# Kernel optimization log

Measured on AMD Instinct MI355X. Metric: run time of the kernel, lower is better.

Reference implementation:

```python
import jax, jax.numpy as jnp
import numpy as np

USERNUM = 8192
ITEMNUM = 8192
DIM = 256
EPS_NORM = 1e-8   # torch.cosine_similarity default eps
CLAMP_MIN = 1e-6
CLAMP_MAX = 1.0


def setup_inputs() -> dict:
    key = jax.random.key(0)
    ks = jax.random.split(key, 12)
    N = USERNUM + ITEMNUM
    s = 1.0 / np.sqrt(DIM)
    return {
        "A": jax.random.uniform(ks[0], (N, N), dtype=jnp.float32) * (2.0 / N),
        "features": jax.random.normal(ks[1], (N, DIM), dtype=jnp.float32),
        "Wg": jax.random.normal(ks[2], (DIM, DIM), dtype=jnp.float32) * s,
        "bg": jnp.zeros((DIM,), dtype=jnp.float32),
        "uW1": jax.random.normal(ks[3], (DIM, DIM), dtype=jnp.float32) * s,
        "ub1": jnp.zeros((DIM,), dtype=jnp.float32),
        "uW2": jax.random.normal(ks[4], (DIM, DIM), dtype=jnp.float32) * s,
        "ub2": jnp.zeros((DIM,), dtype=jnp.float32),
        "iW1": jax.random.normal(ks[5], (DIM, DIM), dtype=jnp.float32) * s,
        "ib1": jnp.zeros((DIM,), dtype=jnp.float32),
        "iW2": jax.random.normal(ks[6], (DIM, DIM), dtype=jnp.float32) * s,
        "ib2": jnp.zeros((DIM,), dtype=jnp.float32),
    }


def _mlp(h, W1, b1, W2, b2):
    return jax.nn.relu(h @ W1 + b1) @ W2 + b2


def reference(A, features, Wg, bg, uW1, ub1, uW2, ub2, iW1, ib1, iW2, ib2):
    # GCN layer: relu(A @ X @ W + b)  -> [N, DIM]
    x = jax.nn.relu((A @ features) @ Wg + bg)
    user = x[:USERNUM]
    item = x[USERNUM:]
    u = _mlp(user, uW1, ub1, uW2, ub2)   # [usernum, DIM]
    it = _mlp(item, iW1, ib1, iW2, ib2)  # [itemnum, DIM]
    # Fused L2-normalize + GEMM replaces the per-row cosine_similarity loop.
    un = u / jnp.maximum(jnp.linalg.norm(u, axis=1, keepdims=True), EPS_NORM)
    itn = it / jnp.maximum(jnp.linalg.norm(it, axis=1, keepdims=True), EPS_NORM)
    sim = un @ itn.T                      # [usernum, itemnum]
    return jnp.clip(sim, CLAMP_MIN, CLAMP_MAX)
```

## Files before the change

### kernel.cpp

```cpp
#include <hip/hip_runtime.h>
#include <hip/hip_bf16.h>

using f32x4 = __attribute__((ext_vector_type(4))) float;
using s16x8 = __attribute__((ext_vector_type(8))) short;
using i32x4 = __attribute__((ext_vector_type(4))) int;

#define NTOT 16384
#define NUSER 8192
#define DIM 256

__device__ __forceinline__ unsigned short f2bf(float f) {
  union { float f; unsigned u; } v; v.f = f;
  unsigned r = v.u + 0x7FFFu + ((v.u >> 16) & 1u);
  return (unsigned short)(r >> 16);
}

__device__ __forceinline__ unsigned pack2bf(float x, float y) {
  float2 t; t.x = x; t.y = y;
  __hip_bfloat162 h = __float22bfloat162_rn(t);
  union { __hip_bfloat162 h; unsigned u; } cv; cv.h = h;
  return cv.u;
}

__device__ __forceinline__ void gload_lds16(const void* g, void* l) {
  __builtin_amdgcn_global_load_lds(
      (const __attribute__((address_space(1))) unsigned int*)g,
      (__attribute__((address_space(3))) unsigned int*)l, 16, 0, 0);
}

__global__ __launch_bounds__(256) void transpose_cvt(const float* __restrict__ src,
                                                     unsigned short* __restrict__ dst,
                                                     int K, int N) {
  __shared__ float tile[64][65];
  const int k0 = blockIdx.x * 64, n0 = blockIdx.y * 64;
  const int t = threadIdx.x;
#pragma unroll
  for (int i = 0; i < 16; i++) {
    int idx = i * 256 + t, r = idx >> 6, c = idx & 63;
    tile[r][c] = src[(size_t)(k0 + r) * N + n0 + c];
  }
  __syncthreads();
#pragma unroll
  for (int i = 0; i < 16; i++) {
    int idx = i * 256 + t, r = idx >> 6, c = idx & 63;
    dst[(size_t)(n0 + r) * K + k0 + c] = f2bf(tile[c][r]);
  }
}

__global__ __launch_bounds__(256) void transpose_w5(const float* __restrict__ w0,
                                                    const float* __restrict__ w1,
                                                    const float* __restrict__ w2,
                                                    const float* __restrict__ w3,
                                                    const float* __restrict__ w4,
                                                    unsigned short* __restrict__ dstbase) {
  __shared__ float tile[64][65];
  const float* srcs[5] = {w0, w1, w2, w3, w4};
  const float* src = srcs[blockIdx.z];
  unsigned short* dst = dstbase + (size_t)blockIdx.z * 65536;
  const int k0 = blockIdx.x * 64, n0 = blockIdx.y * 64;
  const int t = threadIdx.x;
#pragma unroll
  for (int i = 0; i < 16; i++) {
    int idx = i * 256 + t, r = idx >> 6, c = idx & 63;
    tile[r][c] = src[(size_t)(k0 + r) * 256 + n0 + c];
  }
  __syncthreads();
#pragma unroll
  for (int i = 0; i < 16; i++) {
    int idx = i * 256 + t, r = idx >> 6, c = idx & 63;
    dst[(size_t)(n0 + r) * 256 + k0 + c] = f2bf(tile[c][r]);
  }
}

__global__ __launch_bounds__(512) void gemm1(const float* __restrict__ A,
                                             const unsigned short* __restrict__ Ft,
                                             float* __restrict__ F1p) {
  __shared__ char smem[144 * 1024];
  char* const Ab0 = smem;
  char* const Ab1 = smem + 16 * 1024;
  char* const Ab2 = smem + 32 * 1024;
  char* const Bb0 = smem + 48 * 1024;
  char* const Bb1 = smem + 80 * 1024;
  char* const Bb2 = smem + 112 * 1024;

  const int tid = threadIdx.x;
  const int l = tid & 63, w = tid >> 6;
  const int wm = w >> 2, wn = w & 3;
  const int lr = l & 15, lk = l >> 4;

  const int lin = blockIdx.x;
  const int xcd = lin & 7, slot = lin >> 3;
  const int ks = xcd >> 2;
  const int mblk = (xcd & 3) * 32 + slot;
  const int m0 = mblk * 128;
  const size_t ks0 = (size_t)ks * 8192;
  float* out = F1p + (size_t)ks * NTOT * DIM;

  const int arow = tid >> 4, ac16 = tid & 15;
  const float* asrc = A + (size_t)(m0 + arow) * NTOT + ks0 + ac16 * 4;
  int aoff[4];
#pragma unroll
  for (int j = 0; j < 4; j++) {
    int r = j * 32 + arow;
    aoff[j] = r * 128 + ((ac16 * 8) ^ ((r & 7) << 4));
  }

  const int brin = l >> 3;
  const int bldso = w * 4096;
  const char* bsrc = (const char*)Ft + (size_t)(w * 32 + brin) * (NTOT * 2) +
                     ks0 * 2 + (((l & 7) * 16) ^ (brin << 4));

  f32x4 zero = {0.f, 0.f, 0.f, 0.f};
  f32x4 acc[4][4];
#pragma unroll
  for (int i = 0; i < 4; i++)
#pragma unroll
    for (int j = 0; j < 4; j++) acc[i][j] = zero;

  struct AQuad { f32x4 v[4]; };
  AQuad av0, av1, av2;

  auto issueB = [&](int t, char* Bb) {
#pragma unroll
    for (int i = 0; i < 4; i++)
      gload_lds16(bsrc + (size_t)i * 8 * (NTOT * 2) + t * 128,
                  Bb + bldso + i * 1024);
  };
  auto loadA = [&](int t, AQuad& s) {
#pragma unroll
    for (int j = 0; j < 4; j++)
      s.v[j] = __builtin_nontemporal_load(
          (const f32x4*)(asrc + (size_t)j * 32 * NTOT + t * 64));
  };
  auto writeA = [&](const AQuad& s, char* Ab) {
#pragma unroll
    for (int j = 0; j < 4; j++) {
      unsigned lo = pack2bf(s.v[j].x, s.v[j].y);
      unsigned hi = pack2bf(s.v[j].z, s.v[j].w);
      *(unsigned long long*)(Ab + aoff[j]) =
          (unsigned long long)lo | ((unsigned long long)hi << 32);
    }
  };
  auto compute = [&](const char* Ab, const char* Bb) {
#pragma unroll
    for (int kh = 0; kh < 2; kh++) {
      s16x8 af[4], bf[4];
#pragma unroll
      for (int mt = 0; mt < 4; mt++) {
        int r = wm * 64 + mt * 16 + lr;
        int off = r * 128 + ((kh * 64 + lk * 16) ^ ((r & 7) << 4));
        af[mt] = *(const s16x8*)(Ab + off);
      }
#pragma unroll
      for (int nt = 0; nt < 4; nt++) {
        int n = wn * 64 + nt * 16 + lr;
        int off = n * 128 + ((kh * 64 + lk * 16) ^ ((n & 7) << 4));
        bf[nt] = *(const s16x8*)(Bb + off);
      }
#pragma unroll
      for (int mt = 0; mt < 4; mt++)
#pragma unroll
        for (int nt = 0; nt < 4; nt++)
          acc[mt][nt] = __builtin_amdgcn_mfma_f32_16x16x32_bf16(af[mt], bf[nt],
                                                                acc[mt][nt], 0, 0, 0);
    }
  };

#define STEP_BAR(N)                                                \
  asm volatile("s_waitcnt vmcnt(" #N ") lgkmcnt(0)" ::: "memory"); \
  __builtin_amdgcn_s_barrier();                                    \
  __builtin_amdgcn_sched_barrier(0);

  issueB(0, Bb0);
  loadA(0, av0);
  issueB(1, Bb1);
  loadA(1, av1);
  writeA(av0, Ab0);
  STEP_BAR(8)

  for (int t = 0; t < 126; t += 3) {
    issueB(t + 2, Bb2);
    loadA(t + 2, av2);
    compute(Ab0, Bb0);
    writeA(av1, Ab1);
    STEP_BAR(8)
    issueB(t + 3, Bb0);
    loadA(t + 3, av0);
    compute(Ab1, Bb1);
    writeA(av2, Ab2);
    STEP_BAR(8)
    issueB(t + 4, Bb1);
    loadA(t + 4, av1);
    compute(Ab2, Bb2);
    writeA(av0, Ab0);
    STEP_BAR(8)
  }
  compute(Ab0, Bb0);
  writeA(av1, Ab1);
  STEP_BAR(0)
  compute(Ab1, Bb1);
#undef STEP_BAR

#pragma unroll
  for (int mt = 0; mt < 4; mt++) {
    int rbase = m0 + wm * 64 + mt * 16 + lk * 4;
#pragma unroll
    for (int nt = 0; nt < 4; nt++) {
      int c = wn * 64 + nt * 16 + lr;
#pragma unroll
      for (int j = 0; j < 4; j++)
        __builtin_nontemporal_store(acc[mt][nt][j],
                                    out + (size_t)(rbase + j) * DIM + c);
    }
  }
}

__global__ __launch_bounds__(512) void mlp_in(const float* __restrict__ P,
                                              const unsigned short* __restrict__ WT,
                                              const float* __restrict__ bias,
                                              unsigned short* __restrict__ out) {
  __shared__ char smem[40 * 1024];
  char* Ab = smem;
  char* Bb = smem + 8 * 1024;
  const int tid = threadIdx.x, l = tid & 63, w = tid >> 6;
  const int wm = w >> 2, wn = w & 3;
  const int m0 = blockIdx.x * 64;
  const int arow = tid >> 4, ac4 = tid & 15;
  const int bn = tid >> 3, bg = tid & 7;
  const int lr = l & 15, lk = l >> 4;

  f32x4 zero = {0.f, 0.f, 0.f, 0.f};
  f32x4 acc[2][4];
#pragma unroll
  for (int i = 0; i < 2; i++)
#pragma unroll
    for (int j = 0; j < 4; j++) acc[i][j] = zero;

  for (int step = 0; step < 4; step++) {
#pragma unroll
    for (int i = 0; i < 2; i++) {
      int r = i * 32 + arow;
      size_t gi = (size_t)(m0 + r) * DIM + step * 64 + ac4 * 4;
      f32x4 v = *(const f32x4*)(P + gi);
      v += *(const f32x4*)(P + (size_t)NTOT * DIM + gi);
      unsigned lo = pack2bf(v.x, v.y);
      unsigned hi = pack2bf(v.z, v.w);
      int off = (r * 128 + ac4 * 8) ^ ((r & 7) << 4);
      *(unsigned long long*)(Ab + off) =
          (unsigned long long)lo | ((unsigned long long)hi << 32);
    }
#pragma unroll
    for (int i = 0; i < 4; i++) {
      int n = i * 64 + bn;
      i32x4 v = *(const i32x4*)(WT + (size_t)n * DIM + step * 64 + bg * 8);
      int off = (n * 128 + bg * 16) ^ ((n & 7) << 4);
      *(i32x4*)(Bb + off) = v;
    }
    __syncthreads();
#pragma unroll
    for (int kh = 0; kh < 2; kh++) {
      s16x8 af[2], bfr[4];
#pragma unroll
      for (int mt = 0; mt < 2; mt++) {
        int r = wm * 32 + mt * 16 + lr;
        int off = (r * 128 + kh * 64 + lk * 16) ^ ((r & 7) << 4);
        af[mt] = *(const s16x8*)(Ab + off);
      }
#pragma unroll
      for (int nt = 0; nt < 4; nt++) {
        int n = wn * 64 + nt * 16 + lr;
        int off = (n * 128 + kh * 64 + lk * 16) ^ ((n & 7) << 4);
        bfr[nt] = *(const s16x8*)(Bb + off);
      }
#pragma unroll
      for (int mt = 0; mt < 2; mt++)
#pragma unroll
        for (int nt = 0; nt < 4; nt++)
          acc[mt][nt] = __builtin_amdgcn_mfma_f32_16x16x32_bf16(af[mt], bfr[nt],
                                                                acc[mt][nt], 0, 0, 0);
    }
    __syncthreads();
  }
#pragma unroll
  for (int nt = 0; nt < 4; nt++) {
    int c = wn * 64 + nt * 16 + lr;
    float b = bias[c];
#pragma unroll
    for (int mt = 0; mt < 2; mt++) {
      int rbase = m0 + wm * 32 + mt * 16 + lk * 4;
#pragma unroll
      for (int j = 0; j < 4; j++) {
        float v = fmaxf(acc[mt][nt][j] + b, 0.f);
        out[(size_t)(rbase + j) * DIM + c] = f2bf(v);
      }
    }
  }
}

__global__ __launch_bounds__(512) void mlp_hidden(const unsigned short* __restrict__ X,
                                                  const unsigned short* __restrict__ WTu,
                                                  const unsigned short* __restrict__ WTi,
                                                  const float* __restrict__ bu,
                                                  const float* __restrict__ bi,
                                                  unsigned short* __restrict__ out) {
  __shared__ char smem[40 * 1024];
  char* Ab = smem;
  char* Bb = smem + 8 * 1024;
  const int tid = threadIdx.x, l = tid & 63, w = tid >> 6;
  const int wm = w >> 2, wn = w & 3;
  const int m0 = blockIdx.x * 64;
  const unsigned short* WT = (m0 < NUSER) ? WTu : WTi;
  const float* bias = (m0 < NUSER) ? bu : bi;
  const int ar = tid >> 3, ag = tid & 7;
  const int bn = tid >> 3, bg = tid & 7;
  const int lr = l & 15, lk = l >> 4;

  f32x4 zero = {0.f, 0.f, 0.f, 0.f};
  f32x4 acc[2][4];
#pragma unroll
  for (int i = 0; i < 2; i++)
#pragma unroll
    for (int j = 0; j < 4; j++) acc[i][j] = zero;

  for (int step = 0; step < 4; step++) {
    {
      i32x4 v = *(const i32x4*)(X + (size_t)(m0 + ar) * DIM + step * 64 + ag * 8);
      int off = (ar * 128 + ag * 16) ^ ((ar & 7) << 4);
      *(i32x4*)(Ab + off) = v;
    }
#pragma unroll
    for (int i = 0; i < 4; i++) {
      int n = i * 64 + bn;
      i32x4 v = *(const i32x4*)(WT + (size_t)n * DIM + step * 64 + bg * 8);
      int off = (n * 128 + bg * 16) ^ ((n & 7) << 4);
      *(i32x4*)(Bb + off) = v;
    }
    __syncthreads();
#pragma unroll
    for (int kh = 0; kh < 2; kh++) {
      s16x8 af[2], bfr[4];
#pragma unroll
      for (int mt = 0; mt < 2; mt++) {
        int r = wm * 32 + mt * 16 + lr;
        int off = (r * 128 + kh * 64 + lk * 16) ^ ((r & 7) << 4);
        af[mt] = *(const s16x8*)(Ab + off);
      }
#pragma unroll
      for (int nt = 0; nt < 4; nt++) {
        int n = wn * 64 + nt * 16 + lr;
        int off = (n * 128 + kh * 64 + lk * 16) ^ ((n & 7) << 4);
        bfr[nt] = *(const s16x8*)(Bb + off);
      }
#pragma unroll
      for (int mt = 0; mt < 2; mt++)
#pragma unroll
        for (int nt = 0; nt < 4; nt++)
          acc[mt][nt] = __builtin_amdgcn_mfma_f32_16x16x32_bf16(af[mt], bfr[nt],
                                                                acc[mt][nt], 0, 0, 0);
    }
    __syncthreads();
  }
#pragma unroll
  for (int nt = 0; nt < 4; nt++) {
    int c = wn * 64 + nt * 16 + lr;
    float b = bias[c];
#pragma unroll
    for (int mt = 0; mt < 2; mt++) {
      int rbase = m0 + wm * 32 + mt * 16 + lk * 4;
#pragma unroll
      for (int j = 0; j < 4; j++) {
        float v = fmaxf(acc[mt][nt][j] + b, 0.f);
        out[(size_t)(rbase + j) * DIM + c] = f2bf(v);
      }
    }
  }
}

__global__ __launch_bounds__(512) void mlp_out_norm(const unsigned short* __restrict__ H,
                                                    const unsigned short* __restrict__ WTu,
                                                    const unsigned short* __restrict__ WTi,
                                                    const float* __restrict__ bu,
                                                    const float* __restrict__ bi,
                                                    unsigned short* __restrict__ un) {
  __shared__ char smem[40 * 1024];
  __shared__ float rs[64][4];
  char* Ab = smem;
  char* Bb = smem + 8 * 1024;
  const int tid = threadIdx.x, l = tid & 63, w = tid >> 6;
  const int wm = w >> 2, wn = w & 3;
  const int m0 = blockIdx.x * 64;
  const unsigned short* WT = (m0 < NUSER) ? WTu : WTi;
  const float* bias = (m0 < NUSER) ? bu : bi;
  const int ar = tid >> 3, ag = tid & 7;
  const int bn = tid >> 3, bg = tid & 7;
  const int lr = l & 15, lk = l >> 4;

  f32x4 zero = {0.f, 0.f, 0.f, 0.f};
  f32x4 acc[2][4];
#pragma unroll
  for (int i = 0; i < 2; i++)
#pragma unroll
    for (int j = 0; j < 4; j++) acc[i][j] = zero;

  for (int step = 0; step < 4; step++) {
    {
      i32x4 v = *(const i32x4*)(H + (size_t)(m0 + ar) * DIM + step * 64 + ag * 8);
      int off = (ar * 128 + ag * 16) ^ ((ar & 7) << 4);
      *(i32x4*)(Ab + off) = v;
    }
#pragma unroll
    for (int i = 0; i < 4; i++) {
      int n = i * 64 + bn;
      i32x4 v = *(const i32x4*)(WT + (size_t)n * DIM + step * 64 + bg * 8);
      int off = (n * 128 + bg * 16) ^ ((n & 7) << 4);
      *(i32x4*)(Bb + off) = v;
    }
    __syncthreads();
#pragma unroll
    for (int kh = 0; kh < 2; kh++) {
      s16x8 af[2], bfr[4];
#pragma unroll
      for (int mt = 0; mt < 2; mt++) {
        int r = wm * 32 + mt * 16 + lr;
        int off = (r * 128 + kh * 64 + lk * 16) ^ ((r & 7) << 4);
        af[mt] = *(const s16x8*)(Ab + off);
      }
#pragma unroll
      for (int nt = 0; nt < 4; nt++) {
        int n = wn * 64 + nt * 16 + lr;
        int off = (n * 128 + kh * 64 + lk * 16) ^ ((n & 7) << 4);
        bfr[nt] = *(const s16x8*)(Bb + off);
      }
#pragma unroll
      for (int mt = 0; mt < 2; mt++)
#pragma unroll
        for (int nt = 0; nt < 4; nt++)
          acc[mt][nt] = __builtin_amdgcn_mfma_f32_16x16x32_bf16(af[mt], bfr[nt],
                                                                acc[mt][nt], 0, 0, 0);
    }
    __syncthreads();
  }

  float uval[2][4][4];
  float p[2][4];
#pragma unroll
  for (int mt = 0; mt < 2; mt++)
#pragma unroll
    for (int j = 0; j < 4; j++) p[mt][j] = 0.f;
#pragma unroll
  for (int nt = 0; nt < 4; nt++) {
    int c = wn * 64 + nt * 16 + lr;
    float b = bias[c];
#pragma unroll
    for (int mt = 0; mt < 2; mt++)
#pragma unroll
      for (int j = 0; j < 4; j++) {
        float v = acc[mt][nt][j] + b;
        uval[mt][nt][j] = v;
        p[mt][j] += v * v;
      }
  }
#pragma unroll
  for (int d = 1; d < 16; d <<= 1)
#pragma unroll
    for (int mt = 0; mt < 2; mt++)
#pragma unroll
      for (int j = 0; j < 4; j++) p[mt][j] += __shfl_xor(p[mt][j], d, 64);
  if (lr == 0) {
#pragma unroll
    for (int mt = 0; mt < 2; mt++)
#pragma unroll
      for (int j = 0; j < 4; j++) rs[wm * 32 + mt * 16 + lk * 4 + j][wn] = p[mt][j];
  }
  __syncthreads();
#pragma unroll
  for (int mt = 0; mt < 2; mt++) {
    int rl = wm * 32 + mt * 16 + lk * 4;
#pragma unroll
    for (int j = 0; j < 4; j++) {
      float tot = rs[rl + j][0] + rs[rl + j][1] + rs[rl + j][2] + rs[rl + j][3];
      float inv = 1.f / fmaxf(sqrtf(tot), 1e-8f);
#pragma unroll
      for (int nt = 0; nt < 4; nt++) {
        int c = wn * 64 + nt * 16 + lr;
        un[(size_t)(m0 + rl + j) * DIM + c] = f2bf(uval[mt][nt][j] * inv);
      }
    }
  }
}

__global__ __launch_bounds__(512) void simk(const unsigned short* __restrict__ UN,
                                            float* __restrict__ out) {
  __shared__ char smem[128 * 1024];
  char* Ab = smem;
  char* Bb = smem + 64 * 1024;
  const int tid = threadIdx.x, l = tid & 63, w = tid >> 6;
  const int wm = w >> 2, wn = w & 3;
  const int lin = blockIdx.x + (blockIdx.y << 6);
  const int xcd = lin & 7, slot = lin >> 3;
  const int nblk = xcd * 8 + (slot & 7);
  const int mblk = slot >> 3;
  const int m0 = mblk * 128, n0 = nblk * 128;
  const int lr = l & 15, lk = l >> 4;
  const int sr = tid >> 5, sg = tid & 31;

#pragma unroll
  for (int i = 0; i < 8; i++) {
    int r = i * 16 + sr;
    i32x4 va = *(const i32x4*)(UN + (size_t)(m0 + r) * DIM + sg * 8);
    i32x4 vb = *(const i32x4*)(UN + (size_t)(NUSER + n0 + r) * DIM + sg * 8);
    int off = (r * 512 + sg * 16) ^ ((r & 7) << 4);
    *(i32x4*)(Ab + off) = va;
    *(i32x4*)(Bb + off) = vb;
  }
  __syncthreads();

  f32x4 zero = {0.f, 0.f, 0.f, 0.f};
  f32x4 acc[4][2];
#pragma unroll
  for (int i = 0; i < 4; i++)
#pragma unroll
    for (int j = 0; j < 2; j++) acc[i][j] = zero;

#pragma unroll
  for (int ks = 0; ks < 8; ks++) {
    s16x8 af[4], bfr[2];
#pragma unroll
    for (int mt = 0; mt < 4; mt++) {
      int r = wm * 64 + mt * 16 + lr;
      int off = (r * 512 + ks * 64 + lk * 16) ^ ((r & 7) << 4);
      af[mt] = *(const s16x8*)(Ab + off);
    }
#pragma unroll
    for (int nt = 0; nt < 2; nt++) {
      int n = wn * 32 + nt * 16 + lr;
      int off = (n * 512 + ks * 64 + lk * 16) ^ ((n & 7) << 4);
      bfr[nt] = *(const s16x8*)(Bb + off);
    }
#pragma unroll
    for (int mt = 0; mt < 4; mt++)
#pragma unroll
      for (int nt = 0; nt < 2; nt++)
        acc[mt][nt] = __builtin_amdgcn_mfma_f32_16x16x32_bf16(af[mt], bfr[nt],
                                                              acc[mt][nt], 0, 0, 0);
  }

#pragma unroll
  for (int mt = 0; mt < 4; mt++) {
    int rbase = m0 + wm * 64 + mt * 16 + lk * 4;
#pragma unroll
    for (int nt = 0; nt < 2; nt++) {
      int c = n0 + wn * 32 + nt * 16 + lr;
#pragma unroll
      for (int j = 0; j < 4; j++) {
        float v = fminf(fmaxf(acc[mt][nt][j], 1e-6f), 1.0f);
        __builtin_nontemporal_store(v, out + (size_t)(rbase + j) * 8192 + c);
      }
    }
  }
}

extern "C" void kernel_launch(void* const* d_in, const int* in_sizes, int n_in,
                              void* d_out, int out_size, void* d_ws, size_t ws_size,
                              hipStream_t stream) {
  const float* A    = (const float*)d_in[0];
  const float* feat = (const float*)d_in[1];
  const float* Wg   = (const float*)d_in[2];
  const float* bg   = (const float*)d_in[3];
  const float* uW1  = (const float*)d_in[4];
  const float* ub1  = (const float*)d_in[5];
  const float* uW2  = (const float*)d_in[6];
  const float* ub2  = (const float*)d_in[7];
  const float* iW1  = (const float*)d_in[8];
  const float* ib1  = (const float*)d_in[9];
  const float* iW2  = (const float*)d_in[10];
  const float* ib2  = (const float*)d_in[11];
  float* out = (float*)d_out;
  char* ob = (char*)d_out;

  float*          F1p  = (float*)(ob + 0);
  unsigned short* Ft   = (unsigned short*)(ob + 33554432);
  unsigned short* WT5  = (unsigned short*)(ob + 41943040);
  unsigned short* WgT  = WT5;
  unsigned short* uW1T = WT5 + 1 * 65536;
  unsigned short* uW2T = WT5 + 2 * 65536;
  unsigned short* iW1T = WT5 + 3 * 65536;
  unsigned short* iW2T = WT5 + 4 * 65536;
  unsigned short* Xb   = (unsigned short*)(ob + 41943040 + 655360);
  unsigned short* Hb   = (unsigned short*)(ob + 41943040 + 655360 + 8388608);
  unsigned short* UN   = (unsigned short*)d_ws;

  transpose_cvt<<<dim3(256, 4), 256, 0, stream>>>(feat, Ft, NTOT, DIM);
  transpose_w5<<<dim3(4, 4, 5), 256, 0, stream>>>(Wg, uW1, uW2, iW1, iW2, WT5);

  gemm1<<<dim3(256), 512, 0, stream>>>(A, Ft, F1p);
  mlp_in<<<dim3(256), 512, 0, stream>>>(F1p, WgT, bg, Xb);
  mlp_hidden<<<dim3(256), 512, 0, stream>>>(Xb, uW1T, iW1T, ub1, ib1, Hb);
  mlp_out_norm<<<dim3(256), 512, 0, stream>>>(Hb, uW2T, iW2T, ub2, ib2, UN);
  simk<<<dim3(64, 64), 512, 0, stream>>>(UN, out);
}
```

Before: 326.9 us.

## Restructure gemm1 pipeline to double-buffer wider A chunks with per-step B buffers

Replaces the triple-buffered 64-wide K pipeline in gemm1 with a double-buffered scheme. A is loaded in 128-column chunks (eight vector loads per thread) and converted to bf16 once per two B steps, while B stays double-buffered per 64-column step. Shared memory drops from 144KB to 128KB, and the vmcnt waits and barrier placement change. The A prefetch distance is shorter in steps and more registers are held in flight, which could expose load latency.

```diff
diff --git a/kernel.cpp b/kernel.cpp
--- a/kernel.cpp
+++ b/kernel.cpp
@@ -72,16 +72,16 @@
   }
 }
 
+struct AChunk { f32x4 v[8]; };
+
 __global__ __launch_bounds__(512) void gemm1(const float* __restrict__ A,
                                              const unsigned short* __restrict__ Ft,
                                              float* __restrict__ F1p) {
-  __shared__ char smem[144 * 1024];
+  __shared__ char smem[128 * 1024];
   char* const Ab0 = smem;
-  char* const Ab1 = smem + 16 * 1024;
-  char* const Ab2 = smem + 32 * 1024;
-  char* const Bb0 = smem + 48 * 1024;
-  char* const Bb1 = smem + 80 * 1024;
-  char* const Bb2 = smem + 112 * 1024;
+  char* const Ab1 = smem + 32 * 1024;
+  char* const Bb0 = smem + 64 * 1024;
+  char* const Bb1 = smem + 96 * 1024;
 
   const int tid = threadIdx.x;
   const int l = tid & 63, w = tid >> 6;
@@ -98,11 +98,13 @@
 
   const int arow = tid >> 4, ac16 = tid & 15;
   const float* asrc = A + (size_t)(m0 + arow) * NTOT + ks0 + ac16 * 4;
-  int aoff[4];
+  int aoffb[4][2];
 #pragma unroll
   for (int j = 0; j < 4; j++) {
     int r = j * 32 + arow;
-    aoff[j] = r * 128 + ((ac16 * 8) ^ ((r & 7) << 4));
+#pragma unroll
+    for (int c = 0; c < 2; c++)
+      aoffb[j][c] = r * 256 + ((c * 128 + ac16 * 8) ^ ((r & 7) << 4));
   }
 
   const int brin = l >> 3;
@@ -117,8 +119,7 @@
 #pragma unroll
     for (int j = 0; j < 4; j++) acc[i][j] = zero;
 
-  struct AQuad { f32x4 v[4]; };
-  AQuad av0, av1, av2;
+  AChunk avP, avQ;
 
   auto issueB = [&](int t, char* Bb) {
 #pragma unroll
@@ -126,29 +127,33 @@
       gload_lds16(bsrc + (size_t)i * 8 * (NTOT * 2) + t * 128,
                   Bb + bldso + i * 1024);
   };
-  auto loadA = [&](int t, AQuad& s) {
+  auto issueA = [&](int u, AChunk& s) {
 #pragma unroll
     for (int j = 0; j < 4; j++)
-      s.v[j] = __builtin_nontemporal_load(
-          (const f32x4*)(asrc + (size_t)j * 32 * NTOT + t * 64));
+#pragma unroll
+      for (int c = 0; c < 2; c++)
+        s.v[j * 2 + c] = __builtin_nontemporal_load(
+            (const f32x4*)(asrc + (size_t)j * 32 * NTOT + u * 128 + c * 64));
   };
-  auto writeA = [&](const AQuad& s, char* Ab) {
-#pragma unroll
-    for (int j = 0; j < 4; j++) {
-      unsigned lo = pack2bf(s.v[j].x, s.v[j].y);
-      unsigned hi = pack2bf(s.v[j].z, s.v[j].w);
-      *(unsigned long long*)(Ab + aoff[j]) =
-          (unsigned long long)lo | ((unsigned long long)hi << 32);
-    }
+  auto writeA = [&](const AChunk& s, char* Ab) {
+#pragma unroll
+    for (int j = 0; j < 4; j++)
+#pragma unroll
+      for (int c = 0; c < 2; c++) {
+        unsigned lo = pack2bf(s.v[j * 2 + c].x, s.v[j * 2 + c].y);
+        unsigned hi = pack2bf(s.v[j * 2 + c].z, s.v[j * 2 + c].w);
+        *(unsigned long long*)(Ab + aoffb[j][c]) =
+            (unsigned long long)lo | ((unsigned long long)hi << 32);
+      }
   };
-  auto compute = [&](const char* Ab, const char* Bb) {
+  auto computeStep = [&](const char* Ab, int h, const char* Bb) {
 #pragma unroll
     for (int kh = 0; kh < 2; kh++) {
       s16x8 af[4], bf[4];
 #pragma unroll
       for (int mt = 0; mt < 4; mt++) {
         int r = wm * 64 + mt * 16 + lr;
-        int off = r * 128 + ((kh * 64 + lk * 16) ^ ((r & 7) << 4));
+        int off = r * 256 + ((h * 128 + kh * 64 + lk * 16) ^ ((r & 7) << 4));
         af[mt] = *(const s16x8*)(Ab + off);
       }
 #pragma unroll
@@ -166,40 +171,47 @@
     }
   };
 
-#define STEP_BAR(N)                                                \
+#define BAR_V(N)                                                   \
   asm volatile("s_waitcnt vmcnt(" #N ") lgkmcnt(0)" ::: "memory"); \
   __builtin_amdgcn_s_barrier();                                    \
   __builtin_amdgcn_sched_barrier(0);
 
+  issueA(0, avP);
   issueB(0, Bb0);
-  loadA(0, av0);
-  issueB(1, Bb1);
-  loadA(1, av1);
-  writeA(av0, Ab0);
-  STEP_BAR(8)
-
-  for (int t = 0; t < 126; t += 3) {
-    issueB(t + 2, Bb2);
-    loadA(t + 2, av2);
-    compute(Ab0, Bb0);
-    writeA(av1, Ab1);
-    STEP_BAR(8)
-    issueB(t + 3, Bb0);
-    loadA(t + 3, av0);
-    compute(Ab1, Bb1);
-    writeA(av2, Ab2);
-    STEP_BAR(8)
-    issueB(t + 4, Bb1);
-    loadA(t + 4, av1);
-    compute(Ab2, Bb2);
-    writeA(av0, Ab0);
-    STEP_BAR(8)
-  }
-  compute(Ab0, Bb0);
-  writeA(av1, Ab1);
-  STEP_BAR(0)
-  compute(Ab1, Bb1);
-#undef STEP_BAR
+  writeA(avP, Ab0);
+  issueA(1, avQ);
+  BAR_V(8)
+
+  for (int u = 0; u < 62; u += 2) {
+    issueB(2 * u + 1, Bb1);
+    writeA(avQ, Ab1);
+    issueA(u + 2, avP);
+    computeStep(Ab0, 0, Bb0);
+    BAR_V(8)
+    issueB(2 * u + 2, Bb0);
+    computeStep(Ab0, 1, Bb1);
+    BAR_V(0)
+    issueB(2 * u + 3, Bb1);
+    writeA(avP, Ab0);
+    issueA(u + 3, avQ);
+    computeStep(Ab1, 0, Bb0);
+    BAR_V(8)
+    issueB(2 * u + 4, Bb0);
+    computeStep(Ab1, 1, Bb1);
+    BAR_V(0)
+  }
+  issueB(125, Bb1);
+  writeA(avQ, Ab1);
+  computeStep(Ab0, 0, Bb0);
+  BAR_V(0)
+  issueB(126, Bb0);
+  computeStep(Ab0, 1, Bb1);
+  BAR_V(0)
+  issueB(127, Bb1);
+  computeStep(Ab1, 0, Bb0);
+  BAR_V(0)
+  computeStep(Ab1, 1, Bb1);
+#undef BAR_V
 
 #pragma unroll
   for (int mt = 0; mt < 4; mt++) {
```

Result: slower. 360.0 us (+10.1%).

## Fuse GCN projection and both MLP layers into one LDS-resident kernel

Applied to the files above, without the earlier changes.

Merges the three per-row-block GEMM kernels (Wg projection, MLP hidden, MLP output with normalization) into a single kernel. Each 64-row activation tile stays in shared memory between stages, which removes two kernel launches and the global bf16 round trips for the intermediate X and H buffers. In exchange the kernel uses about 97KB of LDS per block, which limits occupancy, and each block still streams all three weight matrices serially. Only 256 blocks run, so the three stages execute back to back without cross-block overlap.

```diff
diff --git a/kernel.cpp b/kernel.cpp
--- a/kernel.cpp
+++ b/kernel.cpp
@@ -215,28 +215,37 @@
   }
 }
 
-__global__ __launch_bounds__(512) void mlp_in(const float* __restrict__ P,
-                                              const unsigned short* __restrict__ WT,
-                                              const float* __restrict__ bias,
-                                              unsigned short* __restrict__ out) {
-  __shared__ char smem[40 * 1024];
-  char* Ab = smem;
-  char* Bb = smem + 8 * 1024;
+__global__ __launch_bounds__(512) void mlp_fused(const float* __restrict__ P,
+                                                 const unsigned short* __restrict__ WgT,
+                                                 const float* __restrict__ bg,
+                                                 const unsigned short* __restrict__ uW1T,
+                                                 const unsigned short* __restrict__ iW1T,
+                                                 const float* __restrict__ ub1,
+                                                 const float* __restrict__ ib1,
+                                                 const unsigned short* __restrict__ uW2T,
+                                                 const unsigned short* __restrict__ iW2T,
+                                                 const float* __restrict__ ub2,
+                                                 const float* __restrict__ ib2,
+                                                 unsigned short* __restrict__ un) {
+  __shared__ char smem[96 * 1024];
+  char* const Xa = smem;
+  char* const Xb = smem + 32 * 1024;
+  char* const Bb = smem + 64 * 1024;
+  __shared__ float rs[64][4];
+
   const int tid = threadIdx.x, l = tid & 63, w = tid >> 6;
   const int wm = w >> 2, wn = w & 3;
   const int m0 = blockIdx.x * 64;
+  const unsigned short* W1 = (m0 < NUSER) ? uW1T : iW1T;
+  const float* b1 = (m0 < NUSER) ? ub1 : ib1;
+  const unsigned short* W2 = (m0 < NUSER) ? uW2T : iW2T;
+  const float* b2 = (m0 < NUSER) ? ub2 : ib2;
   const int arow = tid >> 4, ac4 = tid & 15;
-  const int bn = tid >> 3, bg = tid & 7;
+  const int bn = tid >> 3, bg_ = tid & 7;
   const int lr = l & 15, lk = l >> 4;
 
-  f32x4 zero = {0.f, 0.f, 0.f, 0.f};
-  f32x4 acc[2][4];
-#pragma unroll
-  for (int i = 0; i < 2; i++)
-#pragma unroll
-    for (int j = 0; j < 4; j++) acc[i][j] = zero;
-
-  for (int step = 0; step < 4; step++) {
+#pragma unroll
+  for (int step = 0; step < 4; step++)
 #pragma unroll
     for (int i = 0; i < 2; i++) {
       int r = i * 32 + arow;
@@ -245,212 +254,91 @@
       v += *(const f32x4*)(P + (size_t)NTOT * DIM + gi);
       unsigned lo = pack2bf(v.x, v.y);
       unsigned hi = pack2bf(v.z, v.w);
-      int off = (r * 128 + ac4 * 8) ^ ((r & 7) << 4);
-      *(unsigned long long*)(Ab + off) =
+      int off = r * 512 + ((step * 128 + ac4 * 8) ^ ((r & 7) << 4));
+      *(unsigned long long*)(Xa + off) =
           (unsigned long long)lo | ((unsigned long long)hi << 32);
     }
-#pragma unroll
-    for (int i = 0; i < 4; i++) {
-      int n = i * 64 + bn;
-      i32x4 v = *(const i32x4*)(WT + (size_t)n * DIM + step * 64 + bg * 8);
-      int off = (n * 128 + bg * 16) ^ ((n & 7) << 4);
-      *(i32x4*)(Bb + off) = v;
-    }
-    __syncthreads();
-#pragma unroll
-    for (int kh = 0; kh < 2; kh++) {
-      s16x8 af[2], bfr[4];
+
+  f32x4 zero = {0.f, 0.f, 0.f, 0.f};
+  f32x4 acc[2][4];
+
+  auto phase = [&](const char* Alds, const unsigned short* WT) {
+#pragma unroll
+    for (int i = 0; i < 2; i++)
+#pragma unroll
+      for (int j = 0; j < 4; j++) acc[i][j] = zero;
+    for (int step = 0; step < 4; step++) {
+#pragma unroll
+      for (int i = 0; i < 4; i++) {
+        int n = i * 64 + bn;
+        i32x4 v = *(const i32x4*)(WT + (size_t)n * DIM + step * 64 + bg_ * 8);
+        int off = (n * 128 + bg_ * 16) ^ ((n & 7) << 4);
+        *(i32x4*)(Bb + off) = v;
+      }
+      __syncthreads();
+#pragma unroll
+      for (int kh = 0; kh < 2; kh++) {
+        s16x8 af[2], bfr[4];
+#pragma unroll
+        for (int mt = 0; mt < 2; mt++) {
+          int r = wm * 32 + mt * 16 + lr;
+          int off = r * 512 + ((step * 128 + kh * 64 + lk * 16) ^ ((r & 7) << 4));
+          af[mt] = *(const s16x8*)(Alds + off);
+        }
+#pragma unroll
+        for (int nt = 0; nt < 4; nt++) {
+          int n = wn * 64 + nt * 16 + lr;
+          int off = (n * 128 + kh * 64 + lk * 16) ^ ((n & 7) << 4);
+          bfr[nt] = *(const s16x8*)(Bb + off);
+        }
+#pragma unroll
+        for (int mt = 0; mt < 2; mt++)
+#pragma unroll
+          for (int nt = 0; nt < 4; nt++)
+            acc[mt][nt] = __builtin_amdgcn_mfma_f32_16x16x32_bf16(af[mt], bfr[nt],
+                                                                  acc[mt][nt], 0, 0, 0);
+      }
+      __syncthreads();
+    }
+  };
+  auto reluToLds = [&](const float* bias, char* dst) {
+#pragma unroll
+    for (int nt = 0; nt < 4; nt++) {
+      int c = wn * 64 + nt * 16 + lr;
+      float b = bias[c];
 #pragma unroll
       for (int mt = 0; mt < 2; mt++) {
-        int r = wm * 32 + mt * 16 + lr;
-        int off = (r * 128 + kh * 64 + lk * 16) ^ ((r & 7) << 4);
-        af[mt] = *(const s16x8*)(Ab + off);
-      }
-#pragma unroll
-      for (int nt = 0; nt < 4; nt++) {
-        int n = wn * 64 + nt * 16 + lr;
-        int off = (n * 128 + kh * 64 + lk * 16) ^ ((n & 7) << 4);
-        bfr[nt] = *(const s16x8*)(Bb + off);
-      }
-#pragma unroll
-      for (int mt = 0; mt < 2; mt++)
-#pragma unroll
-        for (int nt = 0; nt < 4; nt++)
-          acc[mt][nt] = __builtin_amdgcn_mfma_f32_16x16x32_bf16(af[mt], bfr[nt],
-                                                                acc[mt][nt], 0, 0, 0);
-    }
-    __syncthreads();
-  }
+        int rbase = wm * 32 + mt * 16 + lk * 4;
+#pragma unroll
+        for (int j = 0; j < 4; j++) {
+          float v = fmaxf(acc[mt][nt][j] + b, 0.f);
+          int row = rbase + j;
+          int off = row * 512 + ((c * 2) ^ ((row & 7) << 4));
+          *(unsigned short*)(dst + off) = f2bf(v);
+        }
+      }
+    }
+  };
+
+  __syncthreads();
+  phase(Xa, WgT);
+  reluToLds(bg, Xb);
+  __syncthreads();
+  phase(Xb, W1);
+  reluToLds(b1, Xa);
+  __syncthreads();
+  phase(Xa, W2);
+
+  float uval[2][4][4];
+  float p[2][4];
+#pragma unroll
+  for (int mt = 0; mt < 2; mt++)
+#pragma unroll
+    for (int j = 0; j < 4; j++) p[mt][j] = 0.f;
 #pragma unroll
   for (int nt = 0; nt < 4; nt++) {
     int c = wn * 64 + nt * 16 + lr;
-    float b = bias[c];
-#pragma unroll
-    for (int mt = 0; mt < 2; mt++) {
-      int rbase = m0 + wm * 32 + mt * 16 + lk * 4;
-#pragma unroll
-      for (int j = 0; j < 4; j++) {
-        float v = fmaxf(acc[mt][nt][j] + b, 0.f);
-        out[(size_t)(rbase + j) * DIM + c] = f2bf(v);
-      }
-    }
-  }
-}
-
-__global__ __launch_bounds__(512) void mlp_hidden(const unsigned short* __restrict__ X,
-                                                  const unsigned short* __restrict__ WTu,
-                                                  const unsigned short* __restrict__ WTi,
-                                                  const float* __restrict__ bu,
-                                                  const float* __restrict__ bi,
-                                                  unsigned short* __restrict__ out) {
-  __shared__ char smem[40 * 1024];
-  char* Ab = smem;
-  char* Bb = smem + 8 * 1024;
-  const int tid = threadIdx.x, l = tid & 63, w = tid >> 6;
-  const int wm = w >> 2, wn = w & 3;
-  const int m0 = blockIdx.x * 64;
-  const unsigned short* WT = (m0 < NUSER) ? WTu : WTi;
-  const float* bias = (m0 < NUSER) ? bu : bi;
-  const int ar = tid >> 3, ag = tid & 7;
-  const int bn = tid >> 3, bg = tid & 7;
-  const int lr = l & 15, lk = l >> 4;
-
-  f32x4 zero = {0.f, 0.f, 0.f, 0.f};
-  f32x4 acc[2][4];
-#pragma unroll
-  for (int i = 0; i < 2; i++)
-#pragma unroll
-    for (int j = 0; j < 4; j++) acc[i][j] = zero;
-
-  for (int step = 0; step < 4; step++) {
-    {
-      i32x4 v = *(const i32x4*)(X + (size_t)(m0 + ar) * DIM + step * 64 + ag * 8);
-      int off = (ar * 128 + ag * 16) ^ ((ar & 7) << 4);
-      *(i32x4*)(Ab + off) = v;
-    }
-#pragma unroll
-    for (int i = 0; i < 4; i++) {
-      int n = i * 64 + bn;
-      i32x4 v = *(const i32x4*)(WT + (size_t)n * DIM + step * 64 + bg * 8);
-      int off = (n * 128 + bg * 16) ^ ((n & 7) << 4);
-      *(i32x4*)(Bb + off) = v;
-    }
-    __syncthreads();
-#pragma unroll
-    for (int kh = 0; kh < 2; kh++) {
-      s16x8 af[2], bfr[4];
-#pragma unroll
-      for (int mt = 0; mt < 2; mt++) {
-        int r = wm * 32 + mt * 16 + lr;
-        int off = (r * 128 + kh * 64 + lk * 16) ^ ((r & 7) << 4);
-        af[mt] = *(const s16x8*)(Ab + off);
-      }
-#pragma unroll
-      for (int nt = 0; nt < 4; nt++) {
-        int n = wn * 64 + nt * 16 + lr;
-        int off = (n * 128 + kh * 64 + lk * 16) ^ ((n & 7) << 4);
-        bfr[nt] = *(const s16x8*)(Bb + off);
-      }
-#pragma unroll
-      for (int mt = 0; mt < 2; mt++)
-#pragma unroll
-        for (int nt = 0; nt < 4; nt++)
-          acc[mt][nt] = __builtin_amdgcn_mfma_f32_16x16x32_bf16(af[mt], bfr[nt],
-                                                                acc[mt][nt], 0, 0, 0);
-    }
-    __syncthreads();
-  }
-#pragma unroll
-  for (int nt = 0; nt < 4; nt++) {
-    int c = wn * 64 + nt * 16 + lr;
-    float b = bias[c];
-#pragma unroll
-    for (int mt = 0; mt < 2; mt++) {
-      int rbase = m0 + wm * 32 + mt * 16 + lk * 4;
-#pragma unroll
-      for (int j = 0; j < 4; j++) {
-        float v = fmaxf(acc[mt][nt][j] + b, 0.f);
-        out[(size_t)(rbase + j) * DIM + c] = f2bf(v);
-      }
-    }
-  }
-}
-
-__global__ __launch_bounds__(512) void mlp_out_norm(const unsigned short* __restrict__ H,
-                                                    const unsigned short* __restrict__ WTu,
-                                                    const unsigned short* __restrict__ WTi,
-                                                    const float* __restrict__ bu,
-                                                    const float* __restrict__ bi,
-                                                    unsigned short* __restrict__ un) {
-  __shared__ char smem[40 * 1024];
-  __shared__ float rs[64][4];
-  char* Ab = smem;
-  char* Bb = smem + 8 * 1024;
-  const int tid = threadIdx.x, l = tid & 63, w = tid >> 6;
-  const int wm = w >> 2, wn = w & 3;
-  const int m0 = blockIdx.x * 64;
-  const unsigned short* WT = (m0 < NUSER) ? WTu : WTi;
-  const float* bias = (m0 < NUSER) ? bu : bi;
-  const int ar = tid >> 3, ag = tid & 7;
-  const int bn = tid >> 3, bg = tid & 7;
-  const int lr = l & 15, lk = l >> 4;
-
-  f32x4 zero = {0.f, 0.f, 0.f, 0.f};
-  f32x4 acc[2][4];
-#pragma unroll
-  for (int i = 0; i < 2; i++)
-#pragma unroll
-    for (int j = 0; j < 4; j++) acc[i][j] = zero;
-
-  for (int step = 0; step < 4; step++) {
-    {
-      i32x4 v = *(const i32x4*)(H + (size_t)(m0 + ar) * DIM + step * 64 + ag * 8);
-      int off = (ar * 128 + ag * 16) ^ ((ar & 7) << 4);
-      *(i32x4*)(Ab + off) = v;
-    }
-#pragma unroll
-    for (int i = 0; i < 4; i++) {
-      int n = i * 64 + bn;
-      i32x4 v = *(const i32x4*)(WT + (size_t)n * DIM + step * 64 + bg * 8);
-      int off = (n * 128 + bg * 16) ^ ((n & 7) << 4);
-      *(i32x4*)(Bb + off) = v;
-    }
-    __syncthreads();
-#pragma unroll
-    for (int kh = 0; kh < 2; kh++) {
-      s16x8 af[2], bfr[4];
-#pragma unroll
-      for (int mt = 0; mt < 2; mt++) {
-        int r = wm * 32 + mt * 16 + lr;
-        int off = (r * 128 + kh * 64 + lk * 16) ^ ((r & 7) << 4);
-        af[mt] = *(const s16x8*)(Ab + off);
-      }
-#pragma unroll
-      for (int nt = 0; nt < 4; nt++) {
-        int n = wn * 64 + nt * 16 + lr;
-        int off = (n * 128 + kh * 64 + lk * 16) ^ ((n & 7) << 4);
-        bfr[nt] = *(const s16x8*)(Bb + off);
-      }
-#pragma unroll
-      for (int mt = 0; mt < 2; mt++)
-#pragma unroll
-        for (int nt = 0; nt < 4; nt++)
-          acc[mt][nt] = __builtin_amdgcn_mfma_f32_16x16x32_bf16(af[mt], bfr[nt],
-                                                                acc[mt][nt], 0, 0, 0);
-    }
-    __syncthreads();
-  }
-
-  float uval[2][4][4];
-  float p[2][4];
-#pragma unroll
-  for (int mt = 0; mt < 2; mt++)
-#pragma unroll
-    for (int j = 0; j < 4; j++) p[mt][j] = 0.f;
-#pragma unroll
-  for (int nt = 0; nt < 4; nt++) {
-    int c = wn * 64 + nt * 16 + lr;
-    float b = bias[c];
+    float b = b2[c];
 #pragma unroll
     for (int mt = 0; mt < 2; mt++)
 #pragma unroll
@@ -586,16 +474,13 @@
   unsigned short* uW2T = WT5 + 2 * 65536;
   unsigned short* iW1T = WT5 + 3 * 65536;
   unsigned short* iW2T = WT5 + 4 * 65536;
-  unsigned short* Xb   = (unsigned short*)(ob + 41943040 + 655360);
-  unsigned short* Hb   = (unsigned short*)(ob + 41943040 + 655360 + 8388608);
   unsigned short* UN   = (unsigned short*)d_ws;
 
   transpose_cvt<<<dim3(256, 4), 256, 0, stream>>>(feat, Ft, NTOT, DIM);
   transpose_w5<<<dim3(4, 4, 5), 256, 0, stream>>>(Wg, uW1, uW2, iW1, iW2, WT5);
 
   gemm1<<<dim3(256), 512, 0, stream>>>(A, Ft, F1p);
-  mlp_in<<<dim3(256), 512, 0, stream>>>(F1p, WgT, bg, Xb);
-  mlp_hidden<<<dim3(256), 512, 0, stream>>>(Xb, uW1T, iW1T, ub1, ib1, Hb);
-  mlp_out_norm<<<dim3(256), 512, 0, stream>>>(Hb, uW2T, iW2T, ub2, ib2, UN);
+  mlp_fused<<<dim3(256), 512, 0, stream>>>(F1p, WgT, bg, uW1T, iW1T, ub1, ib1,
+                                           uW2T, iW2T, ub2, ib2, UN);
   simk<<<dim3(64, 64), 512, 0, stream>>>(UN, out);
 }
```

Result: no change. 320.7 us (median of 2 runs) (-1.9%).
